# Kernel optimization log

Measured on AMD Instinct MI355X. Metric: run time of the kernel, lower is better.

Reference implementation:

```python
import jax, jax.numpy as jnp
import numpy as np

N_NODES = 50000
N_EDGES = 800000
D = 64
IN_DIM = 100
N_GRAPHS = 512
N_LAYERS = 3
OUT_DIM = 24  # n_lbs * n_tasks
BN_EPS = 1e-5


def setup_inputs() -> dict:
    key = jax.random.key(0)
    ks = iter(jax.random.split(key, 40))

    def w(shape):
        fan_in = shape[0]
        return jax.random.normal(next(ks), shape, jnp.float32) / np.float32(np.sqrt(fan_in))

    inp = {}
    inp["x"] = jax.random.normal(next(ks), (N_NODES, IN_DIM), jnp.float32)
    inp["edge_index"] = jax.random.randint(next(ks), (2, N_EDGES), 0, N_NODES, jnp.int32)
    inp["batch"] = jnp.sort(jax.random.randint(next(ks), (N_NODES,), 0, N_GRAPHS, jnp.int32))

    dims_in = [IN_DIM, D, D]
    for i in range(N_LAYERS):
        inp[f"w1_{i}"] = w((dims_in[i], D))
        inp[f"b1_{i}"] = jnp.zeros((D,), jnp.float32)
        inp[f"w2_{i}"] = w((D, D))
        inp[f"b2_{i}"] = jnp.zeros((D,), jnp.float32)

    inp["jk_w"] = w((N_LAYERS * D, D))
    inp["jk_b"] = jnp.zeros((D,), jnp.float32)
    inp["ffn_w1"] = w((D, D))
    inp["ffn_b1"] = jnp.zeros((D,), jnp.float32)
    inp["bn_g"] = jnp.ones((D,), jnp.float32)
    inp["bn_b"] = jnp.zeros((D,), jnp.float32)
    inp["bn_m"] = 0.1 * jax.random.normal(next(ks), (D,), jnp.float32)
    inp["bn_v"] = jax.random.uniform(next(ks), (D,), jnp.float32, 0.5, 1.5)
    inp["ffn_w2"] = w((D, D))
    inp["ffn_b2"] = jnp.zeros((D,), jnp.float32)
    inp["out_w"] = w((D, OUT_DIM))
    inp["out_b"] = jnp.zeros((OUT_DIM,), jnp.float32)
    return inp


def _gin_conv(h, src, dst, w1, b1, w2, b2):
    # sum-aggregate neighbor messages:  agg[dst] += h[src]
    agg = jax.ops.segment_sum(h[src], dst, num_segments=N_NODES)
    z = h + agg  # eps = 0 -> (1 + eps) * x + agg
    # GINConv internal MLP: lin -> relu -> lin (no norm, plain last)
    return jnp.maximum(z @ w1 + b1, 0.0) @ w2 + b2


def reference(x, edge_index, batch,
              w1_0, b1_0, w2_0, b2_0,
              w1_1, b1_1, w2_1, b2_1,
              w1_2, b1_2, w2_2, b2_2,
              jk_w, jk_b,
              ffn_w1, ffn_b1, bn_g, bn_b, bn_m, bn_v, ffn_w2, ffn_b2,
              out_w, out_b):
    src, dst = edge_index[0], edge_index[1]
    layer_params = [(w1_0, b1_0, w2_0, b2_0),
                    (w1_1, b1_1, w2_1, b2_1),
                    (w1_2, b1_2, w2_2, b2_2)]
    xs = []
    h = x
    for (w1, b1, w2, b2) in layer_params:
        h = _gin_conv(h, src, dst, w1, b1, w2, b2)
        h = jnp.maximum(h, 0.0)  # inter-layer ReLU (jk='cat' applies it on every layer)
        xs.append(h)  # dropout is identity in eval
    # JumpingKnowledge 'cat' + final linear -> [N, D]
    h = jnp.concatenate(xs, axis=-1) @ jk_w + jk_b
    # global_add_pool -> [N_GRAPHS, D]
    g = jax.ops.segment_sum(h, batch, num_segments=N_GRAPHS)
    # ffn MLP: lin -> batchnorm (eval, running stats) -> relu -> lin
    t = g @ ffn_w1 + ffn_b1
    t = (t - bn_m) * jax.lax.rsqrt(bn_v + BN_EPS) * bn_g + bn_b
    t = jnp.maximum(t, 0.0) @ ffn_w2 + ffn_b2
    # output layer ('none' uncertainty): plain linear
    logits = t @ out_w + out_b
    return logits
```

## Files before the change

### kernel.cpp

```cpp
#include <hip/hip_runtime.h>

#define NN 50000
#define NE 800000
#define NG 512
#define INDIM 100
#define OUTD 24
#define LROW 72
#define XROW 136
#define CSR_CAP 64
#define B_WPREP 80
#define B_WPREP0 112
#define B_CNT0 308
#define B_GP0 692

typedef __attribute__((ext_vector_type(8))) short short8;
typedef __attribute__((ext_vector_type(4))) float floatx4;

__device__ inline float bf2f(unsigned short u) {
    unsigned v = (unsigned)u << 16;
    float f;
    __builtin_memcpy(&f, &v, 4);
    return f;
}
__device__ inline unsigned short f2bf(float f) {
    unsigned u;
    __builtin_memcpy(&u, &f, 4);
    u += 0x7fffu + ((u >> 16) & 1u);
    return (unsigned short)(u >> 16);
}


__global__ __launch_bounds__(256) void k_prep(const float* __restrict__ s0, const float* __restrict__ s1,
                                              const float* __restrict__ s2, const float* __restrict__ s3,
                                              const float* __restrict__ s4,
                                              const float* __restrict__ w1_0,
                                              unsigned short* __restrict__ wT,
                                              unsigned short* __restrict__ w0T,
                                              int* __restrict__ count,
                                              float* __restrict__ gp) {
    int b = blockIdx.x, tid = threadIdx.x;
    if (b < B_WPREP) {
        const float* srcs[5] = {s0, s1, s2, s3, s4};
        int id = b >> 4;
        int off = ((b & 15) << 8) + tid;
        int k = off >> 6, n = off & 63;
        wT[id * 4096 + n * 64 + k] = f2bf(srcs[id][k * 64 + n]);
    } else if (b < B_WPREP0) {
        int i = (b - B_WPREP) * 256 + tid;
        int n = i >> 7, k = i & 127;
        w0T[n * 128 + k] = (k < INDIM) ? f2bf(w1_0[k * 64 + n]) : 0;
    } else if (b < B_CNT0) {
        int i = (b - B_WPREP0) * 256 + tid;
        if (i < NN) count[i] = 0;
    } else {
        int i = (b - B_CNT0) * 256 + tid;
        if (i < 3 * NG * 64) gp[i] = 0.f;
    }
}


__global__ __launch_bounds__(256) void k_fill(const int* __restrict__ ei,
                                              int* __restrict__ count,
                                              int* __restrict__ csr) {
    unsigned e = blockIdx.x * 256u + threadIdx.x;
    if (e >= NE) return;
    int d = ei[NE + e];
    int s = ei[e];
    int pos = atomicAdd(&count[d], 1);
    if (pos < CSR_CAP) csr[(size_t)d * CSR_CAP + pos] = s;
}


__global__ __launch_bounds__(256) void k_pre0(const float* __restrict__ x,
                                              const unsigned short* __restrict__ w1T,
                                              unsigned short* __restrict__ y) {
    __shared__ __align__(16) unsigned short xs[64 * XROW];
    int tid = threadIdx.x;
    int base = blockIdx.x * 64;
    for (int i = tid; i < 64 * 128; i += 256) {
        int r = i >> 7, c = i & 127;
        int node = base + r;
        float v = (c < INDIM && node < NN) ? x[(size_t)node * INDIM + c] : 0.f;
        xs[r * XROW + c] = f2bf(v);
    }
    __syncthreads();
    int wave = tid >> 6, lane = tid & 63;
    int quad = lane >> 4, l15 = lane & 15;
#pragma unroll
    for (int nt = 0; nt < 4; ++nt) {
        floatx4 c = {0.f, 0.f, 0.f, 0.f};
#pragma unroll
        for (int kk = 0; kk < 4; ++kk) {
            short8 a = *(const short8*)&xs[(wave * 16 + l15) * XROW + kk * 32 + quad * 8];
            short8 bb = *(const short8*)&w1T[(nt * 16 + l15) * 128 + kk * 32 + quad * 8];
            c = __builtin_amdgcn_mfma_f32_16x16x32_bf16(a, bb, c, 0, 0, 0);
        }
        int col = nt * 16 + l15;
#pragma unroll
        for (int r = 0; r < 4; ++r) {
            int row = base + wave * 16 + quad * 4 + r;
            if (row < NN) y[(size_t)row * 64 + col] = f2bf(c[r]);
        }
    }
}


template <bool HAS_NEXT>
__global__ __launch_bounds__(256) void k_layer(const unsigned short* __restrict__ y,
                                               const int* __restrict__ count,
                                               const int* __restrict__ csr,
                                               const float* __restrict__ b1,
                                               const unsigned short* __restrict__ w2T,
                                               const float* __restrict__ b2,
                                               const unsigned short* __restrict__ wnT,
                                               unsigned short* __restrict__ ynext,
                                               const int* __restrict__ batch,
                                               float* __restrict__ gp) {
    __shared__ __align__(16) unsigned short tA[16 * LROW];
    __shared__ __align__(16) unsigned short tB[16 * LROW];
    int wave = threadIdx.x >> 6, lane = threadIdx.x & 63;
    int base = blockIdx.x * 16;
    float bias1 = b1[lane];

    for (int i = 0; i < 4; i += 2) {
        int nA = __builtin_amdgcn_readfirstlane(base + wave * 4 + i);
        int nB = __builtin_amdgcn_readfirstlane(base + wave * 4 + i + 1);
        int cA = min(count[nA], CSR_CAP);
        int cB = min(count[nB], CSR_CAP);
        const int* pA = csr + (size_t)nA * CSR_CAP;
        const int* pB = csr + (size_t)nB * CSR_CAP;
        float aA[4], aB[4];
        aA[0] = bf2f(y[(size_t)nA * 64 + lane]);
        aB[0] = bf2f(y[(size_t)nB * 64 + lane]);
        aA[1] = aA[2] = aA[3] = 0.f;
        aB[1] = aB[2] = aB[3] = 0.f;
        int eA = 0, eB = 0;
        while (eA + 8 <= cA && eB + 8 <= cB) {
            int iA[8], iB[8];
#pragma unroll
            for (int j = 0; j < 8; ++j) { iA[j] = pA[eA + j]; iB[j] = pB[eB + j]; }
            float vA[8], vB[8];
#pragma unroll
            for (int j = 0; j < 8; ++j) vA[j] = bf2f(y[(size_t)iA[j] * 64 + lane]);
#pragma unroll
            for (int j = 0; j < 8; ++j) vB[j] = bf2f(y[(size_t)iB[j] * 64 + lane]);
#pragma unroll
            for (int j = 0; j < 8; ++j) { aA[j & 3] += vA[j]; aB[j & 3] += vB[j]; }
            eA += 8; eB += 8;
        }
        for (; eA + 8 <= cA; eA += 8) {
            int idx[8];
#pragma unroll
            for (int j = 0; j < 8; ++j) idx[j] = pA[eA + j];
#pragma unroll
            for (int j = 0; j < 8; ++j) aA[j & 3] += bf2f(y[(size_t)idx[j] * 64 + lane]);
        }
        if (eA + 4 <= cA) {
            int i0 = pA[eA], i1 = pA[eA + 1], i2 = pA[eA + 2], i3 = pA[eA + 3];
            aA[0] += bf2f(y[(size_t)i0 * 64 + lane]);
            aA[1] += bf2f(y[(size_t)i1 * 64 + lane]);
            aA[2] += bf2f(y[(size_t)i2 * 64 + lane]);
            aA[3] += bf2f(y[(size_t)i3 * 64 + lane]);
            eA += 4;
        }
        if (eA + 2 <= cA) {
            int i0 = pA[eA], i1 = pA[eA + 1];
            aA[0] += bf2f(y[(size_t)i0 * 64 + lane]);
            aA[1] += bf2f(y[(size_t)i1 * 64 + lane]);
            eA += 2;
        }
        if (eA < cA) aA[0] += bf2f(y[(size_t)pA[eA] * 64 + lane]);
        for (; eB + 8 <= cB; eB += 8) {
            int idx[8];
#pragma unroll
            for (int j = 0; j < 8; ++j) idx[j] = pB[eB + j];
#pragma unroll
            for (int j = 0; j < 8; ++j) aB[j & 3] += bf2f(y[(size_t)idx[j] * 64 + lane]);
        }
        if (eB + 4 <= cB) {
            int i0 = pB[eB], i1 = pB[eB + 1], i2 = pB[eB + 2], i3 = pB[eB + 3];
            aB[0] += bf2f(y[(size_t)i0 * 64 + lane]);
            aB[1] += bf2f(y[(size_t)i1 * 64 + lane]);
            aB[2] += bf2f(y[(size_t)i2 * 64 + lane]);
            aB[3] += bf2f(y[(size_t)i3 * 64 + lane]);
            eB += 4;
        }
        if (eB + 2 <= cB) {
            int i0 = pB[eB], i1 = pB[eB + 1];
            aB[0] += bf2f(y[(size_t)i0 * 64 + lane]);
            aB[1] += bf2f(y[(size_t)i1 * 64 + lane]);
            eB += 2;
        }
        if (eB < cB) aB[0] += bf2f(y[(size_t)pB[eB] * 64 + lane]);

        float sA = (aA[0] + aA[1]) + (aA[2] + aA[3]);
        float sB = (aB[0] + aB[1]) + (aB[2] + aB[3]);
        tA[(wave * 4 + i) * LROW + lane]     = f2bf(fmaxf(sA + bias1, 0.f));
        tA[(wave * 4 + i + 1) * LROW + lane] = f2bf(fmaxf(sB + bias1, 0.f));
    }
    __syncthreads();

    int quad = lane >> 4, l15 = lane & 15;

    short8 a_k0 = *(const short8*)&tA[l15 * LROW + quad * 8];
    short8 a_k1 = *(const short8*)&tA[l15 * LROW + 32 + quad * 8];
    {
        int col = wave * 16 + l15;
        short8 b_k0 = *(const short8*)&w2T[col * 64 + quad * 8];
        short8 b_k1 = *(const short8*)&w2T[col * 64 + 32 + quad * 8];
        floatx4 c = {0.f, 0.f, 0.f, 0.f};
        c = __builtin_amdgcn_mfma_f32_16x16x32_bf16(a_k0, b_k0, c, 0, 0, 0);
        c = __builtin_amdgcn_mfma_f32_16x16x32_bf16(a_k1, b_k1, c, 0, 0, 0);
        float bb = b2[col];
#pragma unroll
        for (int r = 0; r < 4; ++r) {
            float h = fmaxf(c[r] + bb, 0.f);
            tB[(quad * 4 + r) * LROW + col] = f2bf(h);
        }
    }
    __syncthreads();

    if (wave == 0) {
        float run = 0.f;
        int curg = batch[base];
        for (int r = 0; r < 16; ++r) {
            int g2 = batch[base + r];
            if (g2 != curg) {
                atomicAdd(&gp[curg * 64 + lane], run);
                run = 0.f;
                curg = g2;
            }
            run += bf2f(tB[r * LROW + lane]);
        }
        atomicAdd(&gp[curg * 64 + lane], run);
    }

    if (HAS_NEXT) {
        short8 h_k0 = *(const short8*)&tB[l15 * LROW + quad * 8];
        short8 h_k1 = *(const short8*)&tB[l15 * LROW + 32 + quad * 8];
        int col = wave * 16 + l15;
        short8 w_k0 = *(const short8*)&wnT[col * 64 + quad * 8];
        short8 w_k1 = *(const short8*)&wnT[col * 64 + 32 + quad * 8];
        floatx4 cy = {0.f, 0.f, 0.f, 0.f};
        cy = __builtin_amdgcn_mfma_f32_16x16x32_bf16(h_k0, w_k0, cy, 0, 0, 0);
        cy = __builtin_amdgcn_mfma_f32_16x16x32_bf16(h_k1, w_k1, cy, 0, 0, 0);
#pragma unroll
        for (int r = 0; r < 4; ++r) {
            int row = base + quad * 4 + r;
            ynext[(size_t)row * 64 + col] = f2bf(cy[r]);
        }
    }
}


__device__ inline int lbound(const int* __restrict__ b, int v) {
    int lo = 0, hi = NN;
    while (lo < hi) {
        int m = (lo + hi) >> 1;
        if (b[m] < v) lo = m + 1; else hi = m;
    }
    return lo;
}

__global__ __launch_bounds__(64) void k_final(const float* __restrict__ gp,
                                              const int* __restrict__ batch,
                                              const float* __restrict__ jkw,
                                              const float* __restrict__ jkb,
                                              const float* __restrict__ w1,
                                              const float* __restrict__ b1,
                                              const float* __restrict__ bng,
                                              const float* __restrict__ bnb,
                                              const float* __restrict__ bnm,
                                              const float* __restrict__ bnv,
                                              const float* __restrict__ w2,
                                              const float* __restrict__ b2,
                                              const float* __restrict__ ow,
                                              const float* __restrict__ ob,
                                              float* __restrict__ out) {
    __shared__ float gs[192];
    __shared__ float gv[64];
    __shared__ float t2[64];
    __shared__ float t3[64];
    int gr = blockIdx.x, lane = threadIdx.x;
    gs[lane]       = gp[0 * NG * 64 + gr * 64 + lane];
    gs[64 + lane]  = gp[1 * NG * 64 + gr * 64 + lane];
    gs[128 + lane] = gp[2 * NG * 64 + gr * 64 + lane];
    float cntf = (float)(lbound(batch, gr + 1) - lbound(batch, gr));
    __syncthreads();
    float acc = cntf * jkb[lane];
#pragma unroll 8
    for (int k = 0; k < 192; ++k) acc = fmaf(gs[k], jkw[k * 64 + lane], acc);
    gv[lane] = acc;
    __syncthreads();
    acc = b1[lane];
#pragma unroll 8
    for (int k = 0; k < 64; ++k) acc = fmaf(gv[k], w1[k * 64 + lane], acc);
    acc = (acc - bnm[lane]) * rsqrtf(bnv[lane] + 1e-5f) * bng[lane] + bnb[lane];
    t2[lane] = fmaxf(acc, 0.f);
    __syncthreads();
    float acc2 = b2[lane];
#pragma unroll 8
    for (int k = 0; k < 64; ++k) acc2 = fmaf(t2[k], w2[k * 64 + lane], acc2);
    t3[lane] = acc2;
    __syncthreads();
    if (lane < OUTD) {
        float acc3 = ob[lane];
#pragma unroll 8
        for (int k = 0; k < 64; ++k) acc3 = fmaf(t3[k], ow[k * OUTD + lane], acc3);
        out[gr * OUTD + lane] = acc3;
    }
}

extern "C" void kernel_launch(void* const* d_in, const int* in_sizes, int n_in,
                              void* d_out, int out_size, void* d_ws, size_t ws_size,
                              hipStream_t stream) {
    const float* x     = (const float*)d_in[0];
    const int*   ei    = (const int*)d_in[1];
    const int*   batch = (const int*)d_in[2];
    const float* w1_0 = (const float*)d_in[3];
    const float* b1_0 = (const float*)d_in[4];
    const float* w2_0 = (const float*)d_in[5];
    const float* b2_0 = (const float*)d_in[6];
    const float* w1_1 = (const float*)d_in[7];
    const float* b1_1 = (const float*)d_in[8];
    const float* w2_1 = (const float*)d_in[9];
    const float* b2_1 = (const float*)d_in[10];
    const float* w1_2 = (const float*)d_in[11];
    const float* b1_2 = (const float*)d_in[12];
    const float* w2_2 = (const float*)d_in[13];
    const float* b2_2 = (const float*)d_in[14];
    const float* jk_w = (const float*)d_in[15];
    const float* jk_b = (const float*)d_in[16];
    const float* ffn_w1 = (const float*)d_in[17];
    const float* ffn_b1 = (const float*)d_in[18];
    const float* bn_g = (const float*)d_in[19];
    const float* bn_b = (const float*)d_in[20];
    const float* bn_m = (const float*)d_in[21];
    const float* bn_v = (const float*)d_in[22];
    const float* ffn_w2 = (const float*)d_in[23];
    const float* ffn_b2 = (const float*)d_in[24];
    const float* out_w  = (const float*)d_in[25];
    const float* out_b  = (const float*)d_in[26];

    float* ws = (float*)d_ws;
    unsigned short* ya = (unsigned short*)ws;
    unsigned short* yb = ya + 3200000;
    float* gp  = (float*)(yb + 3200000);
    int*   count = (int*)(gp + 3 * NG * 64);
    int*   csr   = count + NN;
    unsigned short* wT  = (unsigned short*)(csr + (size_t)NN * CSR_CAP);
    unsigned short* w0T = wT + 5 * 4096;

    k_prep<<<B_GP0, 256, 0, stream>>>(w2_0, w2_1, w2_2, w1_1, w1_2, w1_0,
                                      wT, w0T, count, gp);

    k_fill<<<(NE + 255) / 256, 256, 0, stream>>>(ei, count, csr);
    k_pre0<<<(NN + 63) / 64, 256, 0, stream>>>(x, w0T, ya);

    int nblk = NN / 16;
    k_layer<true><<<nblk, 256, 0, stream>>>(ya, count, csr, b1_0,
                                            wT + 0 * 4096, b2_0, wT + 3 * 4096,
                                            yb, batch, gp + 0 * NG * 64);
    k_layer<true><<<nblk, 256, 0, stream>>>(yb, count, csr, b1_1,
                                            wT + 1 * 4096, b2_1, wT + 4 * 4096,
                                            ya, batch, gp + 1 * NG * 64);
    k_layer<false><<<nblk, 256, 0, stream>>>(ya, count, csr, b1_2,
                                             wT + 2 * 4096, b2_2, nullptr,
                                             nullptr, batch, gp + 2 * NG * 64);

    k_final<<<NG, 64, 0, stream>>>(gp, batch, jk_w, jk_b,
                                   ffn_w1, ffn_b1, bn_g, bn_b, bn_m, bn_v,
                                   ffn_w2, ffn_b2, out_w, out_b, (float*)d_out);
}
```

Measured before the change: 271.7 us.

## Build CSR via two-pass bucketed sort with shared-memory atomics

Replaces the single edge-scatter kernel, which issued one global atomic per edge and wrote randomly into the padded CSR, with a two-pass bucketed scheme. The first pass groups edges by destination bucket (256 nodes per bucket) using LDS atomic counters and one global cursor atomic per bucket per block, writing packed 16-bit dst/src pairs. The second pass has one block per bucket place edges into the CSR with LDS counters and write the per-node counts, so the CSR writes stay within a small address region. The cost is an extra kernel launch and an intermediate pairs buffer. The scheme relies on node ids fitting in 16 bits and on a fixed bucket capacity of 5120 edges.

```diff
diff --git a/kernel.cpp b/kernel.cpp
--- a/kernel.cpp
+++ b/kernel.cpp
@@ -8,6 +8,11 @@
 #define LROW 72
 #define XROW 136
 #define CSR_CAP 64
+#define NB 196
+#define BSH 8
+#define BCAP 5120
+#define CURS 16
+#define EPB 4096
 #define B_WPREP 80
 #define B_WPREP0 112
 #define B_CNT0 308
@@ -37,7 +42,8 @@
                                               unsigned short* __restrict__ wT,
                                               unsigned short* __restrict__ w0T,
                                               int* __restrict__ count,
-                                              float* __restrict__ gp) {
+                                              float* __restrict__ gp,
+                                              int* __restrict__ cursor) {
     int b = blockIdx.x, tid = threadIdx.x;
     if (b < B_WPREP) {
         const float* srcs[5] = {s0, s1, s2, s3, s4};
@@ -52,6 +58,7 @@
     } else if (b < B_CNT0) {
         int i = (b - B_WPREP0) * 256 + tid;
         if (i < NN) count[i] = 0;
+        if (i < NB * CURS) cursor[i] = 0;
     } else {
         int i = (b - B_CNT0) * 256 + tid;
         if (i < 3 * NG * 64) gp[i] = 0.f;
@@ -59,15 +66,69 @@
 }
 
 
-__global__ __launch_bounds__(256) void k_fill(const int* __restrict__ ei,
-                                              int* __restrict__ count,
-                                              int* __restrict__ csr) {
-    unsigned e = blockIdx.x * 256u + threadIdx.x;
-    if (e >= NE) return;
-    int d = ei[NE + e];
-    int s = ei[e];
-    int pos = atomicAdd(&count[d], 1);
-    if (pos < CSR_CAP) csr[(size_t)d * CSR_CAP + pos] = s;
+__global__ __launch_bounds__(256) void k_fill_a(const int* __restrict__ ei,
+                                                int* __restrict__ cursor,
+                                                unsigned* __restrict__ pairs) {
+    __shared__ int lcnt[NB];
+    __shared__ int lbase[NB];
+    int t = threadIdx.x;
+    for (int i = t; i < NB; i += 256) lcnt[i] = 0;
+    __syncthreads();
+    unsigned e0 = blockIdx.x * EPB;
+    unsigned short dv[16], sv[16];
+    short bkt[16];
+#pragma unroll
+    for (int j = 0; j < 16; ++j) {
+        unsigned e = e0 + j * 256u + t;
+        if (e < NE) {
+            int d = ei[NE + e];
+            int s = ei[e];
+            dv[j] = (unsigned short)d;
+            sv[j] = (unsigned short)s;
+            bkt[j] = (short)(d >> BSH);
+            atomicAdd(&lcnt[bkt[j]], 1);
+        } else {
+            bkt[j] = -1;
+        }
+    }
+    __syncthreads();
+    for (int i = t; i < NB; i += 256) {
+        lbase[i] = atomicAdd(&cursor[i * CURS], lcnt[i]);
+        lcnt[i] = 0;
+    }
+    __syncthreads();
+#pragma unroll
+    for (int j = 0; j < 16; ++j) {
+        if (bkt[j] >= 0) {
+            int b = bkt[j];
+            int p = lbase[b] + atomicAdd(&lcnt[b], 1);
+            if (p < BCAP)
+                pairs[(size_t)b * BCAP + p] = ((unsigned)dv[j] << 16) | (unsigned)sv[j];
+        }
+    }
+}
+
+
+__global__ __launch_bounds__(256) void k_fill_b(const unsigned* __restrict__ pairs,
+                                                const int* __restrict__ cursor,
+                                                int* __restrict__ count,
+                                                int* __restrict__ csr) {
+    __shared__ int lcnt[256];
+    int t = threadIdx.x, b = blockIdx.x;
+    lcnt[t] = 0;
+    __syncthreads();
+    int tot = min(cursor[b * CURS], BCAP);
+    const unsigned* pp = pairs + (size_t)b * BCAP;
+    for (int i = t; i < tot; i += 256) {
+        unsigned pr = pp[i];
+        int d = (int)(pr >> 16);
+        int s = (int)(pr & 0xFFFFu);
+        int pos = atomicAdd(&lcnt[d & 255], 1);
+        if (pos < CSR_CAP) csr[(size_t)d * CSR_CAP + pos] = s;
+    }
+    __syncthreads();
+    int node = (b << BSH) + t;
+    if (node < NN) count[node] = lcnt[t];
 }
 
 
@@ -350,11 +411,15 @@
     int*   csr   = count + NN;
     unsigned short* wT  = (unsigned short*)(csr + (size_t)NN * CSR_CAP);
     unsigned short* w0T = wT + 5 * 4096;
+    int* cursor = (int*)(w0T + 64 * 128);
+    unsigned* pairs = (unsigned*)(cursor + NB * CURS);
 
     k_prep<<<B_GP0, 256, 0, stream>>>(w2_0, w2_1, w2_2, w1_1, w1_2, w1_0,
-                                      wT, w0T, count, gp);
-
-    k_fill<<<(NE + 255) / 256, 256, 0, stream>>>(ei, count, csr);
+                                      wT, w0T, count, gp, cursor);
+
+    k_fill_a<<<(NE + EPB - 1) / EPB, 256, 0, stream>>>(ei, cursor, pairs);
+    k_fill_b<<<NB, 256, 0, stream>>>(pairs, cursor, count, csr);
+
     k_pre0<<<(NN + 63) / 64, 256, 0, stream>>>(x, w0T, ya);
 
     int nblk = NN / 16;
```

Result: faster. 248.0 us (-8.7%).

## Build CSR via two-pass bucketed scatter with LDS atomics and merge kernels

Applied to the files above, without the earlier changes.

Replaces the global-atomic CSR fill with a two-pass bucket sort. The first pass groups edges into 256-node buckets per edge block using shared-memory atomics, packing dst and src into 16-bit halves. The second pass places each bucket's edges into the CSR with LDS counters and writes the per-node counts directly, so the count-zeroing pass is no longer needed. The prep/fill and bucket-merge/pre0 kernels are also fused to save launches. Risks: the 16-bit packing only holds for node ids below 65536, and per-segment capping at 64 can silently drop edges on skewed inputs.

```diff
diff --git a/kernel.cpp b/kernel.cpp
--- a/kernel.cpp
+++ b/kernel.cpp
@@ -8,10 +8,15 @@
 #define LROW 72
 #define XROW 136
 #define CSR_CAP 64
+#define NB 196
+#define BSH 8
+#define NFB 196
+#define SEGCAP 64
+#define EPB 4096
 #define B_WPREP 80
 #define B_WPREP0 112
-#define B_CNT0 308
-#define B_GP0 692
+#define B_GPZ 496
+#define B_TOT 692
 
 typedef __attribute__((ext_vector_type(8))) short short8;
 typedef __attribute__((ext_vector_type(4))) float floatx4;
@@ -30,14 +35,17 @@
 }
 
 
-__global__ __launch_bounds__(256) void k_prep(const float* __restrict__ s0, const float* __restrict__ s1,
-                                              const float* __restrict__ s2, const float* __restrict__ s3,
-                                              const float* __restrict__ s4,
-                                              const float* __restrict__ w1_0,
-                                              unsigned short* __restrict__ wT,
-                                              unsigned short* __restrict__ w0T,
-                                              int* __restrict__ count,
-                                              float* __restrict__ gp) {
+__global__ __launch_bounds__(256) void k_prep_fill(const float* __restrict__ s0, const float* __restrict__ s1,
+                                                   const float* __restrict__ s2, const float* __restrict__ s3,
+                                                   const float* __restrict__ s4,
+                                                   const float* __restrict__ w1_0,
+                                                   const int* __restrict__ ei,
+                                                   unsigned short* __restrict__ wT,
+                                                   unsigned short* __restrict__ w0T,
+                                                   float* __restrict__ gp,
+                                                   int* __restrict__ segcnt,
+                                                   unsigned* __restrict__ pairs) {
+    __shared__ int lcnt[NB];
     int b = blockIdx.x, tid = threadIdx.x;
     if (b < B_WPREP) {
         const float* srcs[5] = {s0, s1, s2, s3, s4};
@@ -49,34 +57,66 @@
         int i = (b - B_WPREP) * 256 + tid;
         int n = i >> 7, k = i & 127;
         w0T[n * 128 + k] = (k < INDIM) ? f2bf(w1_0[k * 64 + n]) : 0;
-    } else if (b < B_CNT0) {
+    } else if (b < B_GPZ) {
         int i = (b - B_WPREP0) * 256 + tid;
-        if (i < NN) count[i] = 0;
+        if (i < 3 * NG * 64) gp[i] = 0.f;
     } else {
-        int i = (b - B_CNT0) * 256 + tid;
-        if (i < 3 * NG * 64) gp[i] = 0.f;
-    }
-}
-
-
-__global__ __launch_bounds__(256) void k_fill(const int* __restrict__ ei,
+        int blk = b - B_GPZ;
+        for (int i = tid; i < NB; i += 256) lcnt[i] = 0;
+        __syncthreads();
+        unsigned e0 = (unsigned)blk * EPB;
+#pragma unroll
+        for (int j = 0; j < 16; ++j) {
+            unsigned e = e0 + j * 256u + tid;
+            if (e < NE) {
+                int d = ei[NE + e];
+                int s = ei[e];
+                int bkt = d >> BSH;
+                int pos = atomicAdd(&lcnt[bkt], 1);
+                if (pos < SEGCAP)
+                    pairs[((size_t)blk * NB + bkt) * SEGCAP + pos] =
+                        ((unsigned)(unsigned short)d << 16) | (unsigned)(unsigned short)s;
+            }
+        }
+        __syncthreads();
+        for (int i = tid; i < NB; i += 256)
+            segcnt[blk * NB + i] = min(lcnt[i], SEGCAP);
+    }
+}
+
+
+__global__ __launch_bounds__(256) void k_mid2(const unsigned* __restrict__ pairs,
+                                              const int* __restrict__ segcnt,
                                               int* __restrict__ count,
-                                              int* __restrict__ csr) {
-    unsigned e = blockIdx.x * 256u + threadIdx.x;
-    if (e >= NE) return;
-    int d = ei[NE + e];
-    int s = ei[e];
-    int pos = atomicAdd(&count[d], 1);
-    if (pos < CSR_CAP) csr[(size_t)d * CSR_CAP + pos] = s;
-}
-
-
-__global__ __launch_bounds__(256) void k_pre0(const float* __restrict__ x,
+                                              int* __restrict__ csr,
+                                              const float* __restrict__ x,
                                               const unsigned short* __restrict__ w1T,
                                               unsigned short* __restrict__ y) {
     __shared__ __align__(16) unsigned short xs[64 * XROW];
     int tid = threadIdx.x;
-    int base = blockIdx.x * 64;
+    if (blockIdx.x < NB) {
+        int* lcnt = (int*)xs;
+        int* scnt = lcnt + 256;
+        int b = blockIdx.x;
+        lcnt[tid] = 0;
+        for (int i = tid; i < NB; i += 256) scnt[i] = segcnt[i * NB + b];
+        __syncthreads();
+        for (int i = tid; i < NFB * SEGCAP; i += 256) {
+            int blk = i >> 6, pos = i & (SEGCAP - 1);
+            if (pos < scnt[blk]) {
+                unsigned pr = pairs[((size_t)blk * NB + b) * SEGCAP + pos];
+                int d = (int)(pr >> 16);
+                int s = (int)(pr & 0xFFFFu);
+                int p2 = atomicAdd(&lcnt[d & 255], 1);
+                if (p2 < CSR_CAP) csr[(size_t)d * CSR_CAP + p2] = s;
+            }
+        }
+        __syncthreads();
+        int node = (b << BSH) + tid;
+        if (node < NN) count[node] = lcnt[tid];
+        return;
+    }
+    int base = (blockIdx.x - NB) * 64;
     for (int i = tid; i < 64 * 128; i += 256) {
         int r = i >> 7, c = i & 127;
         int node = base + r;
@@ -350,12 +390,13 @@
     int*   csr   = count + NN;
     unsigned short* wT  = (unsigned short*)(csr + (size_t)NN * CSR_CAP);
     unsigned short* w0T = wT + 5 * 4096;
-
-    k_prep<<<B_GP0, 256, 0, stream>>>(w2_0, w2_1, w2_2, w1_1, w1_2, w1_0,
-                                      wT, w0T, count, gp);
-
-    k_fill<<<(NE + 255) / 256, 256, 0, stream>>>(ei, count, csr);
-    k_pre0<<<(NN + 63) / 64, 256, 0, stream>>>(x, w0T, ya);
+    int* segcnt = (int*)(w0T + 64 * 128);
+    unsigned* pairs = (unsigned*)(segcnt + NFB * NB);
+
+    k_prep_fill<<<B_TOT, 256, 0, stream>>>(w2_0, w2_1, w2_2, w1_1, w1_2, w1_0, ei,
+                                           wT, w0T, gp, segcnt, pairs);
+
+    k_mid2<<<NB + (NN + 63) / 64, 256, 0, stream>>>(pairs, segcnt, count, csr, x, w0T, ya);
 
     int nblk = NN / 16;
     k_layer<true><<<nblk, 256, 0, stream>>>(ya, count, csr, b1_0,
```

New measurement: 246.4 us. -9.3%, faster.
